# Performance work log

Hardware: AMD Instinct MI355X
Metric: run time of the kernel (lower is better)

Reference implementation:

```python
import jax, jax.numpy as jnp
import numpy as np

PATCH = 5
DIM = 256
HEADS = 8
EPS = 1e-5


def split_patches(t, p):
    # t: [B,H,W,C] -> overlapping patches [B,H,W,p,p,C], stride 1, zero-pad p//2
    pad = p // 2
    tp = jnp.pad(t, ((0, 0), (pad, pad), (pad, pad), (0, 0)))
    H, W = t.shape[1], t.shape[2]
    rows = jnp.arange(H)[:, None] + jnp.arange(p)[None, :]  # [H,p]
    cols = jnp.arange(W)[:, None] + jnp.arange(p)[None, :]  # [W,p]
    return tp[:, rows[:, None, :, None], cols[None, :, None, :], :]


def layernorm(v, g, b):
    mu = jnp.mean(v, axis=-1, keepdims=True)
    var = jnp.var(v, axis=-1, keepdims=True)
    return (v - mu) * jax.lax.rsqrt(var + EPS) * g + b


def mha(q, k, v, w, b, mask):
    # w: [4,D,D] stacked (Wq,Wk,Wv,Wo), b: [4,D]; q:[N,Lq,D], k,v:[N,Lk,D]
    N, Lq, D = q.shape
    dh = D // HEADS
    qh = (q @ w[0] + b[0]).reshape(N, Lq, HEADS, dh)
    kh = (k @ w[1] + b[1]).reshape(N, -1, HEADS, dh)
    vh = (v @ w[2] + b[2]).reshape(N, -1, HEADS, dh)
    sc = jnp.einsum('nqhd,nkhd->nhqk', qh, kh) * (1.0 / float(np.sqrt(dh)))
    if mask is not None:
        sc = jnp.where(mask, sc, jnp.asarray(-1e9, sc.dtype))
    a = jax.nn.softmax(sc, axis=-1)
    o = jnp.einsum('nhqk,nkhd->nqhd', a, vh).reshape(N, Lq, D)
    return o @ w[3] + b[3], a


def setup_inputs() -> dict:
    key = jax.random.key(0)
    ks = jax.random.split(key, 10)
    B, H, W, D = 1, 64, 64, DIM
    x = jax.random.normal(ks[0], (B, H, W, D), dtype=jnp.float32)
    memory = jax.random.normal(ks[1], (B, H, W, D), dtype=jnp.float32)
    active_nodes = jax.random.randint(ks[2], (B, H, W), 0, 2).astype(bool)
    s = 0.05
    return {
        'x': x, 'memory': memory, 'active_nodes': active_nodes,
        'attn_w': jax.random.normal(ks[3], (4, D, D), dtype=jnp.float32) * s,
        'attn_b': jnp.zeros((4, D), dtype=jnp.float32),
        'pattn_w': jax.random.normal(ks[4], (4, D, D), dtype=jnp.float32) * s,
        'pattn_b': jnp.zeros((4, D), dtype=jnp.float32),
        'ff_w1': jax.random.normal(ks[5], (D, 2 * D), dtype=jnp.float32) * s,
        'ff_b1': jnp.zeros((2 * D,), dtype=jnp.float32),
        'ff_w2': jax.random.normal(ks[6], (2 * D, D), dtype=jnp.float32) * s,
        'ff_b2': jnp.zeros((D,), dtype=jnp.float32),
        'ln_g': jnp.ones((3, D), dtype=jnp.float32),   # norm1, norm2, norm3
        'ln_b': jnp.zeros((3, D), dtype=jnp.float32),
    }


def reference(x, memory, active_nodes, attn_w, attn_b, pattn_w, pattn_b,
              ff_w1, ff_b1, ff_w2, ff_b2, ln_g, ln_b):
    B, H, W, D = x.shape
    p = PATCH
    center = p // 2
    L = p * p
    cp = L // 2  # flattened center point

    act = active_nodes[..., None]                      # [B,H,W,1] bool
    ap = split_patches(act, p)                         # [B,H,W,p,p,1]
    # faithful to source: zeroes the entire patch at GRID position (center,center)
    ap = ap.at[:, center, center].set(False)
    wo_center = jnp.any(ap.reshape(B, H, W, L, 1), axis=3)  # [B,H,W,1]
    act = jnp.logical_and(wo_center, act)
    ap = split_patches(act, p)                         # recomputed with updated mask

    xp = split_patches(x, p) * ap                      # zero inactive neighbors
    xp = xp.reshape(B, H, W, L, D)
    mp = split_patches(memory, p).reshape(B, H, W, L, D)
    mask = ap[..., 0].reshape(B, H, W, L)

    N = B * H * W
    keys = xp.reshape(N, L, D)
    mem = mp.reshape(N, L, D)
    q = keys[:, cp:cp + 1, :]                          # [N,1,D]
    m = mask.reshape(N, L)[:, None, None, :]           # [N,1,1,L]

    # EncoderLayer (eval mode: dropout = identity)
    s_, attn = mha(q, keys, keys, attn_w, attn_b, m)
    s = layernorm(q + s_, ln_g[0], ln_b[0])            # norm1
    s_, _ = mha(s, mem, mem, pattn_w, pattn_b, None)
    s = layernorm(s + s_, ln_g[2], ln_b[2])            # norm3
    ff = jax.nn.relu(s @ ff_w1 + ff_b1) @ ff_w2 + ff_b2
    s = layernorm(s + ff, ln_g[1], ln_b[1])            # norm2

    out = jnp.where(act, s[:, 0, :].reshape(B, H, W, D), jnp.asarray(0.0, x.dtype))
    return out, act[..., 0]
```

## Files before the change

### kernel.cpp

```cpp
#include <hip/hip_runtime.h>
#include <math.h>

#define D 256
#define H2 512
#define HEADS 8
#define L 25
#define GH 64
#define GW 64
#define NN 4096
#define EPS 1e-5f
#define SCALE 0.17677669529663687f
#define NND 1048576

typedef __attribute__((ext_vector_type(8))) short short8;
typedef __attribute__((ext_vector_type(4))) float f32x4;

__device__ __forceinline__ bool act_at(const int* __restrict__ active, int h, int w) {
    if (h < 0 || h >= GH || w < 0 || w >= GW) return false;
    if (h == 2 && w == 2) return false;
    return active[h * GW + w] != 0;
}

__device__ __forceinline__ unsigned short f2b(float f) {
    unsigned u = __float_as_uint(f);
    u += 0x7fffu + ((u >> 16) & 1u);
    return (unsigned short)(u >> 16);
}
__device__ __forceinline__ float b2f(short v) {
    return __uint_as_float(((unsigned)(unsigned short)v) << 16);
}

__global__ __launch_bounds__(256)
void prep_kernel(const float* __restrict__ x, const float* __restrict__ mem,
                 const int* __restrict__ active,
                 const float* __restrict__ attn_w, const float* __restrict__ pattn_w,
                 const float* __restrict__ ff_w1, const float* __restrict__ ff_w2,
                 const float* __restrict__ pattn_b,
                 unsigned short* __restrict__ xmB, unsigned short* __restrict__ memB,
                 unsigned short* __restrict__ wB,
                 unsigned short* __restrict__ k2bias, unsigned short* __restrict__ v2bias) {
    const int tid = threadIdx.x;
    const int bid = blockIdx.x;
    if (bid < 192) {
        __shared__ float tile[64][65];
        const float* src; unsigned short* dst;
        int i0, n0, srcLen, dstLen;
        if (bid < 128) {
            int mat = bid >> 4, t16 = bid & 15;
            i0 = (t16 >> 2) * 64; n0 = (t16 & 3) * 64;
            src = (mat < 4) ? (attn_w + mat * 65536) : (pattn_w + (mat - 4) * 65536);
            dst = wB + mat * 65536;
            srcLen = 256; dstLen = 256;
        } else if (bid < 160) {
            int t = bid - 128;
            i0 = (t >> 3) * 64; n0 = (t & 7) * 64;
            src = ff_w1; dst = wB + 524288;
            srcLen = 512; dstLen = 256;
        } else {
            int t = bid - 160;
            i0 = (t >> 2) * 64; n0 = (t & 3) * 64;
            src = ff_w2; dst = wB + 655360;
            srcLen = 256; dstLen = 512;
        }
        int c = tid & 63, r4 = tid >> 6;
        for (int rr = 0; rr < 64; rr += 4)
            tile[rr + r4][c] = src[(size_t)(i0 + rr + r4) * srcLen + n0 + c];
        __syncthreads();
        for (int rr = 0; rr < 64; rr += 4) {
            int r = rr + r4;
            dst[(size_t)(n0 + r) * dstLen + i0 + c] = f2b(tile[c][r]);
        }
    } else {
        const int t0 = (bid - 192) * 256 + tid;
        for (int t = t0; t < 524800; t += 512 * 256) {
            if (t < 262144) {
                int n = t >> 6;
                bool a = act_at(active, n >> 6, n & 63);
                float4 v = ((const float4*)x)[t];
                ushort4 u;
                u.x = f2b(a ? v.x : 0.0f); u.y = f2b(a ? v.y : 0.0f);
                u.z = f2b(a ? v.z : 0.0f); u.w = f2b(a ? v.w : 0.0f);
                ((ushort4*)xmB)[t] = u;
            } else if (t < 524288) {
                int tt = t - 262144;
                float4 v = ((const float4*)mem)[tt];
                ushort4 u;
                u.x = f2b(v.x); u.y = f2b(v.y); u.z = f2b(v.z); u.w = f2b(v.w);
                ((ushort4*)memB)[tt] = u;
            } else {
                int tt = t - 524288;
                if (tt < 256) k2bias[tt] = f2b(pattn_b[256 + tt]);
                else          v2bias[tt - 256] = f2b(pattn_b[512 + (tt - 256)]);
            }
        }
    }
}

__global__ __launch_bounds__(256)
void proj_gemm(const unsigned short* __restrict__ xmB,
               const unsigned short* __restrict__ memB,
               const unsigned short* __restrict__ wB,
               const float* __restrict__ attn_b, const float* __restrict__ pattn_b,
               unsigned short* __restrict__ q1b, unsigned short* __restrict__ k1b,
               unsigned short* __restrict__ v1b, unsigned short* __restrict__ k2b,
               unsigned short* __restrict__ v2b) {
    const int s  = blockIdx.y >> 2;
    const int n0 = (blockIdx.y & 3) * 64;
    const unsigned short* A  = (s < 3) ? xmB : memB;
    const int wtIdx = (s < 3) ? s : (s + 2);
    const unsigned short* WT = wB + (size_t)wtIdx * 65536;
    const float* bias = (s < 3) ? (attn_b + s * 256) : (pattn_b + (s - 2) * 256);
    unsigned short* outB;
    switch (s) { case 0: outB = q1b; break; case 1: outB = k1b; break;
                 case 2: outB = v1b; break; case 3: outB = k2b; break;
                 default: outB = v2b; }

    const int tid = threadIdx.x;
    const int wave = tid >> 6, lane = tid & 63;
    const int m0 = blockIdx.x * 64 + wave * 16;
    const int lr = lane & 15;
    const int lk = (lane >> 4) << 3;
    f32x4 acc[4] = {};
    const unsigned short* arow = A  + (size_t)(m0 + lr) * 256 + lk;
    const unsigned short* brow = WT + (size_t)(n0 + lr) * 256 + lk;
    #pragma unroll
    for (int kk = 0; kk < 256; kk += 32) {
        short8 a = *(const short8*)(arow + kk);
        #pragma unroll
        for (int nf = 0; nf < 4; ++nf) {
            short8 b = *(const short8*)(brow + (size_t)nf * 16 * 256 + kk);
            acc[nf] = __builtin_amdgcn_mfma_f32_16x16x32_bf16(a, b, acc[nf], 0, 0, 0);
        }
    }
    const int rbase = m0 + ((lane >> 4) << 2);
    #pragma unroll
    for (int nf = 0; nf < 4; ++nf) {
        int c = n0 + nf * 16 + lr;
        float bc = bias[c];
        #pragma unroll
        for (int jj = 0; jj < 4; ++jj)
            outB[(size_t)(rbase + jj) * 256 + c] = f2b(acc[nf][jj] + bc);
    }
}

#define KV_OFF   0
#define ACT_OFF  51200
#define WGT_OFF  51328
#define REDA_OFF 64128
#define REDB_OFF 64640
#define STAT_OFF 65152
#define SMEM_SZ  65280
#define T1B_OFF  0
#define SB_OFF   8448
#define HB_OFF   16896

__device__ __forceinline__ void load_union(const unsigned short* __restrict__ base,
                                           int h, int w0, int fallback,
                                           unsigned short (*kvU)[256], int tid) {
    for (int c = tid; c < 3200; c += 512) {
        int u = c >> 5, part = c & 31;
        int r = u / 20;
        int hh = h - 2 + r, ww = w0 - 2 + (u - r * 20);
        bool ib = ((unsigned)hh < GH) && ((unsigned)ww < GW);
        int row = ib ? ((hh << 6) | ww) : fallback;
        *(uint4*)&kvU[u][part * 8] = *(const uint4*)(base + (size_t)row * 256 + part * 8);
    }
}

__global__ __launch_bounds__(512)
void fused_kernel(const int* __restrict__ active, const float* __restrict__ x,
                  const unsigned short* __restrict__ wB,
                  const float* __restrict__ attn_b, const float* __restrict__ pattn_b,
                  const float* __restrict__ ff_b1, const float* __restrict__ ff_b2,
                  const float* __restrict__ ln_g, const float* __restrict__ ln_b,
                  const unsigned short* __restrict__ q1b,
                  const unsigned short* __restrict__ k1b,
                  const unsigned short* __restrict__ v1b,
                  const unsigned short* __restrict__ k2b,
                  const unsigned short* __restrict__ v2b,
                  float* __restrict__ out) {
    const int tid = threadIdx.x;
    const int wv = tid >> 6, lane = tid & 63;
    const int lr = lane & 15, qi = lane >> 4;
    const int bid = ((blockIdx.x & 7) << 5) | (blockIdx.x >> 3);
    const int n0 = bid * 16;
    const int h = n0 >> 6, w0 = n0 & 63;
    const int half = lane >> 5, lam = lane & 31;
    const int m = wv * 2 + half;

    __shared__ __align__(16) char smem[SMEM_SZ];
    unsigned short (*kvU)[256] = (unsigned short(*)[256])(smem + KV_OFF);
    unsigned char* actU        = (unsigned char*)(smem + ACT_OFF);
    float (*wgt)[8][25]        = (float(*)[8][25])(smem + WGT_OFF);
    float (*redA)[8]           = (float(*)[8])(smem + REDA_OFF);
    float (*redB)[8]           = (float(*)[8])(smem + REDB_OFF);
    float (*stats)[2]          = (float(*)[2])(smem + STAT_OFF);
    unsigned short (*T1b)[264] = (unsigned short(*)[264])(smem + T1B_OFF);
    unsigned short (*Sb)[264]  = (unsigned short(*)[264])(smem + SB_OFF);
    unsigned short (*Hb)[520]  = (unsigned short(*)[520])(smem + HB_OFF);

    if (tid < 100) {
        int r = tid / 20;
        int hh = h - 2 + r, ww = w0 - 2 + (tid - r * 20);
        actU[tid] = act_at(active, hh, ww) ? 1 : 0;
    }
    load_union(k1b, h, w0, 0, kvU, tid);
    __syncthreads();

    {
        float q[8];
        short8 qv = *(const short8*)(q1b + (size_t)(n0 + m) * 256 + lam * 8);
        #pragma unroll
        for (int j = 0; j < 8; ++j) q[j] = b2f(qv[j]);
        #pragma unroll 5
        for (int l = 0; l < L; ++l) {
            int u = (l / 5) * 20 + m + (l % 5);
            short8 kv = *(const short8*)&kvU[u][lam * 8];
            float p = q[0] * b2f(kv[0]);
            #pragma unroll
            for (int j = 1; j < 8; ++j) p = fmaf(q[j], b2f(kv[j]), p);
            p += __shfl_xor(p, 1); p += __shfl_xor(p, 2);
            float sv = actU[u] ? p * SCALE : -1e30f;
            if ((lam & 3) == 0) wgt[m][lam >> 2][l] = sv;
        }
    }
    __syncthreads();
    if (tid < 128) {
        int mm = tid >> 3, hd = tid & 7;
        float mx = -1e30f;
        for (int l = 0; l < L; ++l) mx = fmaxf(mx, wgt[mm][hd][l]);
        float sum = 0.0f;
        for (int l = 0; l < L; ++l) { float e = expf(wgt[mm][hd][l] - mx); wgt[mm][hd][l] = e; sum += e; }
        float inv = 1.0f / sum;
        for (int l = 0; l < L; ++l) wgt[mm][hd][l] *= inv;
    }
    __syncthreads();
    load_union(v1b, h, w0, 0, kvU, tid);
    __syncthreads();
    {
        float o[8] = {0.f,0.f,0.f,0.f,0.f,0.f,0.f,0.f};
        #pragma unroll 5
        for (int l = 0; l < L; ++l) {
            int u = (l / 5) * 20 + m + (l % 5);
            if (actU[u]) {
                float wt = wgt[m][lam >> 2][l];
                short8 v8 = *(const short8*)&kvU[u][lam * 8];
                #pragma unroll
                for (int j = 0; j < 8; ++j) o[j] = fmaf(wt, b2f(v8[j]), o[j]);
            }
        }
        __syncthreads();
        unsigned short u8[8];
        #pragma unroll
        for (int j = 0; j < 8; ++j) u8[j] = f2b(o[j]);
        *(uint4*)&T1b[m][lam * 8] = *(uint4*)u8;
    }
    __syncthreads();

    float sreg[2][4];
    {
        const unsigned short* Wo1T = wB + 3 * 65536;
        f32x4 acc[2] = {};
        #pragma unroll
        for (int kk = 0; kk < 256; kk += 32) {
            short8 a = *(const short8*)&T1b[lr][qi * 8 + kk];
            #pragma unroll
            for (int nf = 0; nf < 2; ++nf) {
                short8 b = *(const short8*)(Wo1T + (size_t)(wv * 32 + nf * 16 + lr) * 256 + qi * 8 + kk);
                acc[nf] = __builtin_amdgcn_mfma_f32_16x16x32_bf16(a, b, acc[nf], 0, 0, 0);
            }
        }
        float v[2][4], s1[4] = {0.f,0.f,0.f,0.f}, s2[4] = {0.f,0.f,0.f,0.f};
        #pragma unroll
        for (int nf = 0; nf < 2; ++nf) {
            int c = wv * 32 + nf * 16 + lr;
            float bc = attn_b[768 + c];
            #pragma unroll
            for (int jj = 0; jj < 4; ++jj) {
                int row = n0 + qi * 4 + jj;
                float vv = acc[nf][jj] + bc + x[(size_t)row * D + c];
                v[nf][jj] = vv; s1[jj] += vv; s2[jj] += vv * vv;
            }
        }
        #pragma unroll
        for (int jj = 0; jj < 4; ++jj) {
            #pragma unroll
            for (int off = 1; off < 16; off <<= 1) {
                s1[jj] += __shfl_xor(s1[jj], off);
                s2[jj] += __shfl_xor(s2[jj], off);
            }
        }
        if (lr == 0) {
            #pragma unroll
            for (int jj = 0; jj < 4; ++jj) { redA[qi*4+jj][wv] = s1[jj]; redB[qi*4+jj][wv] = s2[jj]; }
        }
        __syncthreads();
        if (tid < 16) {
            float a1 = 0.f, a2 = 0.f;
            #pragma unroll
            for (int q8 = 0; q8 < 8; ++q8) { a1 += redA[tid][q8]; a2 += redB[tid][q8]; }
            float mu = a1 * (1.0f / D);
            float var = a2 * (1.0f / D) - mu * mu;
            stats[tid][0] = mu; stats[tid][1] = rsqrtf(var + EPS);
        }
        __syncthreads();
        #pragma unroll
        for (int nf = 0; nf < 2; ++nf) {
            int c = wv * 32 + nf * 16 + lr;
            float gg = ln_g[c], bb = ln_b[c];
            #pragma unroll
            for (int jj = 0; jj < 4; ++jj) {
                int ridx = qi * 4 + jj;
                float ov = (v[nf][jj] - stats[ridx][0]) * stats[ridx][1] * gg + bb;
                sreg[nf][jj] = ov;
                Sb[ridx][c] = f2b(ov);
            }
        }
    }
    __syncthreads();

    {
        const unsigned short* Wq2T = wB + 4 * 65536;
        f32x4 acc[2] = {};
        #pragma unroll
        for (int kk = 0; kk < 256; kk += 32) {
            short8 a = *(const short8*)&Sb[lr][qi * 8 + kk];
            #pragma unroll
            for (int nf = 0; nf < 2; ++nf) {
                short8 b = *(const short8*)(Wq2T + (size_t)(wv * 32 + nf * 16 + lr) * 256 + qi * 8 + kk);
                acc[nf] = __builtin_amdgcn_mfma_f32_16x16x32_bf16(a, b, acc[nf], 0, 0, 0);
            }
        }
        __syncthreads();
        #pragma unroll
        for (int nf = 0; nf < 2; ++nf) {
            int c = wv * 32 + nf * 16 + lr;
            float bc = pattn_b[c];
            #pragma unroll
            for (int jj = 0; jj < 4; ++jj)
                T1b[qi * 4 + jj][c] = f2b(acc[nf][jj] + bc);
        }
    }
    __syncthreads();

    float q2[8];
    {
        short8 qv = *(const short8*)&T1b[m][lam * 8];
        #pragma unroll
        for (int j = 0; j < 8; ++j) q2[j] = b2f(qv[j]);
    }
    __syncthreads();
    load_union(k2b, h, w0, NN, kvU, tid);
    __syncthreads();

    #pragma unroll 5
    for (int l = 0; l < L; ++l) {
        int u = (l / 5) * 20 + m + (l % 5);
        short8 kv = *(const short8*)&kvU[u][lam * 8];
        float p = q2[0] * b2f(kv[0]);
        #pragma unroll
        for (int j = 1; j < 8; ++j) p = fmaf(q2[j], b2f(kv[j]), p);
        p += __shfl_xor(p, 1); p += __shfl_xor(p, 2);
        if ((lam & 3) == 0) wgt[m][lam >> 2][l] = p * SCALE;
    }
    __syncthreads();
    if (tid < 128) {
        int mm = tid >> 3, hd = tid & 7;
        float mx = -1e30f;
        for (int l = 0; l < L; ++l) mx = fmaxf(mx, wgt[mm][hd][l]);
        float sum = 0.0f;
        for (int l = 0; l < L; ++l) { float e = expf(wgt[mm][hd][l] - mx); wgt[mm][hd][l] = e; sum += e; }
        float inv = 1.0f / sum;
        for (int l = 0; l < L; ++l) wgt[mm][hd][l] *= inv;
    }
    __syncthreads();
    load_union(v2b, h, w0, NN, kvU, tid);
    __syncthreads();
    {
        float o[8] = {0.f,0.f,0.f,0.f,0.f,0.f,0.f,0.f};
        #pragma unroll 5
        for (int l = 0; l < L; ++l) {
            int u = (l / 5) * 20 + m + (l % 5);
            float wt = wgt[m][lam >> 2][l];
            short8 v8 = *(const short8*)&kvU[u][lam * 8];
            #pragma unroll
            for (int j = 0; j < 8; ++j) o[j] = fmaf(wt, b2f(v8[j]), o[j]);
        }
        __syncthreads();
        unsigned short u8[8];
        #pragma unroll
        for (int j = 0; j < 8; ++j) u8[j] = f2b(o[j]);
        *(uint4*)&T1b[m][lam * 8] = *(uint4*)u8;
    }
    __syncthreads();

    float s2reg[2][4];
    {
        const unsigned short* Wo2T = wB + 7 * 65536;
        f32x4 acc[2] = {};
        #pragma unroll
        for (int kk = 0; kk < 256; kk += 32) {
            short8 a = *(const short8*)&T1b[lr][qi * 8 + kk];
            #pragma unroll
            for (int nf = 0; nf < 2; ++nf) {
                short8 b = *(const short8*)(Wo2T + (size_t)(wv * 32 + nf * 16 + lr) * 256 + qi * 8 + kk);
                acc[nf] = __builtin_amdgcn_mfma_f32_16x16x32_bf16(a, b, acc[nf], 0, 0, 0);
            }
        }
        float v[2][4], s1[4] = {0.f,0.f,0.f,0.f}, s2[4] = {0.f,0.f,0.f,0.f};
        #pragma unroll
        for (int nf = 0; nf < 2; ++nf) {
            int c = wv * 32 + nf * 16 + lr;
            float bc = pattn_b[768 + c];
            #pragma unroll
            for (int jj = 0; jj < 4; ++jj) {
                float vv = acc[nf][jj] + bc + sreg[nf][jj];
                v[nf][jj] = vv; s1[jj] += vv; s2[jj] += vv * vv;
            }
        }
        #pragma unroll
        for (int jj = 0; jj < 4; ++jj) {
            #pragma unroll
            for (int off = 1; off < 16; off <<= 1) {
                s1[jj] += __shfl_xor(s1[jj], off);
                s2[jj] += __shfl_xor(s2[jj], off);
            }
        }
        if (lr == 0) {
            #pragma unroll
            for (int jj = 0; jj < 4; ++jj) { redA[qi*4+jj][wv] = s1[jj]; redB[qi*4+jj][wv] = s2[jj]; }
        }
        __syncthreads();
        if (tid < 16) {
            float a1 = 0.f, a2 = 0.f;
            #pragma unroll
            for (int q8 = 0; q8 < 8; ++q8) { a1 += redA[tid][q8]; a2 += redB[tid][q8]; }
            float mu = a1 * (1.0f / D);
            float var = a2 * (1.0f / D) - mu * mu;
            stats[tid][0] = mu; stats[tid][1] = rsqrtf(var + EPS);
        }
        __syncthreads();
        #pragma unroll
        for (int nf = 0; nf < 2; ++nf) {
            int c = wv * 32 + nf * 16 + lr;
            float gg = ln_g[512 + c], bb = ln_b[512 + c];
            #pragma unroll
            for (int jj = 0; jj < 4; ++jj) {
                int ridx = qi * 4 + jj;
                float ov = (v[nf][jj] - stats[ridx][0]) * stats[ridx][1] * gg + bb;
                s2reg[nf][jj] = ov;
                Sb[ridx][c] = f2b(ov);
            }
        }
    }
    __syncthreads();

    {
        const unsigned short* W1T = wB + 524288;
        f32x4 acc[4] = {};
        #pragma unroll
        for (int kk = 0; kk < 256; kk += 32) {
            short8 a = *(const short8*)&Sb[lr][qi * 8 + kk];
            #pragma unroll
            for (int nf = 0; nf < 4; ++nf) {
                short8 b = *(const short8*)(W1T + (size_t)(wv * 64 + nf * 16 + lr) * 256 + qi * 8 + kk);
                acc[nf] = __builtin_amdgcn_mfma_f32_16x16x32_bf16(a, b, acc[nf], 0, 0, 0);
            }
        }
        #pragma unroll
        for (int nf = 0; nf < 4; ++nf) {
            int c = wv * 64 + nf * 16 + lr;
            float bc = ff_b1[c];
            #pragma unroll
            for (int jj = 0; jj < 4; ++jj)
                Hb[qi * 4 + jj][c] = f2b(fmaxf(acc[nf][jj] + bc, 0.0f));
        }
    }
    __syncthreads();

    {
        const unsigned short* W2T = wB + 655360;
        f32x4 acc[2] = {};
        #pragma unroll
        for (int kk = 0; kk < 512; kk += 32) {
            short8 a = *(const short8*)&Hb[lr][qi * 8 + kk];
            #pragma unroll
            for (int nf = 0; nf < 2; ++nf) {
                short8 b = *(const short8*)(W2T + (size_t)(wv * 32 + nf * 16 + lr) * 512 + qi * 8 + kk);
                acc[nf] = __builtin_amdgcn_mfma_f32_16x16x32_bf16(a, b, acc[nf], 0, 0, 0);
            }
        }
        float v[2][4], s1[4] = {0.f,0.f,0.f,0.f}, s2[4] = {0.f,0.f,0.f,0.f};
        #pragma unroll
        for (int nf = 0; nf < 2; ++nf) {
            int c = wv * 32 + nf * 16 + lr;
            float bc = ff_b2[c];
            #pragma unroll
            for (int jj = 0; jj < 4; ++jj) {
                float vv = acc[nf][jj] + bc + s2reg[nf][jj];
                v[nf][jj] = vv; s1[jj] += vv; s2[jj] += vv * vv;
            }
        }
        #pragma unroll
        for (int jj = 0; jj < 4; ++jj) {
            #pragma unroll
            for (int off = 1; off < 16; off <<= 1) {
                s1[jj] += __shfl_xor(s1[jj], off);
                s2[jj] += __shfl_xor(s2[jj], off);
            }
        }
        if (lr == 0) {
            #pragma unroll
            for (int jj = 0; jj < 4; ++jj) { redA[qi*4+jj][wv] = s1[jj]; redB[qi*4+jj][wv] = s2[jj]; }
        }
        __syncthreads();
        if (tid < 16) {
            float a1 = 0.f, a2 = 0.f;
            #pragma unroll
            for (int q8 = 0; q8 < 8; ++q8) { a1 += redA[tid][q8]; a2 += redB[tid][q8]; }
            float mu = a1 * (1.0f / D);
            float var = a2 * (1.0f / D) - mu * mu;
            stats[tid][0] = mu; stats[tid][1] = rsqrtf(var + EPS);
        }
        __syncthreads();
        bool arow_act[4];
        #pragma unroll
        for (int jj = 0; jj < 4; ++jj) {
            int row = n0 + qi * 4 + jj;
            arow_act[jj] = act_at(active, row >> 6, row & 63);
        }
        #pragma unroll
        for (int nf = 0; nf < 2; ++nf) {
            int c = wv * 32 + nf * 16 + lr;
            float gg = ln_g[256 + c], bb = ln_b[256 + c];
            #pragma unroll
            for (int jj = 0; jj < 4; ++jj) {
                int ridx = qi * 4 + jj;
                float ov = (v[nf][jj] - stats[ridx][0]) * stats[ridx][1] * gg + bb;
                out[(size_t)(n0 + ridx) * D + c] = arow_act[jj] ? ov : 0.0f;
            }
        }
        if (tid < 16) {
            int row = n0 + tid;
            out[(size_t)NND + row] = act_at(active, row >> 6, row & 63) ? 1.0f : 0.0f;
        }
    }
}

extern "C" void kernel_launch(void* const* d_in, const int* in_sizes, int n_in,
                              void* d_out, int out_size, void* d_ws, size_t ws_size,
                              hipStream_t stream) {
    const float* x       = (const float*)d_in[0];
    const float* memory  = (const float*)d_in[1];
    const int*   active  = (const int*)d_in[2];
    const float* attn_w  = (const float*)d_in[3];
    const float* attn_b  = (const float*)d_in[4];
    const float* pattn_w = (const float*)d_in[5];
    const float* pattn_b = (const float*)d_in[6];
    const float* ff_w1   = (const float*)d_in[7];
    const float* ff_b1   = (const float*)d_in[8];
    const float* ff_w2   = (const float*)d_in[9];
    const float* ff_b2   = (const float*)d_in[10];
    const float* ln_g    = (const float*)d_in[11];
    const float* ln_b    = (const float*)d_in[12];
    float* out = (float*)d_out;

    unsigned short* wsb = (unsigned short*)d_ws;
    unsigned short* xmB  = wsb;
    unsigned short* memB = wsb + (size_t)NND;
    unsigned short* wB   = wsb + 2 * (size_t)NND;
    unsigned short* q1b  = wB + 786432;
    unsigned short* k1b  = q1b + (size_t)NND;
    unsigned short* v1b  = k1b + (size_t)NND;
    unsigned short* k2b  = v1b + (size_t)NND;
    unsigned short* v2b  = k2b + (size_t)NND + 256;

    hipLaunchKernelGGL(prep_kernel, dim3(704), dim3(256), 0, stream,
                       x, memory, active, attn_w, pattn_w, ff_w1, ff_w2, pattn_b,
                       xmB, memB, wB, k2b + (size_t)NND, v2b + (size_t)NND);
    hipLaunchKernelGGL(proj_gemm, dim3(64, 20), dim3(256), 0, stream,
                       xmB, memB, wB, attn_b, pattn_b, q1b, k1b, v1b, k2b, v2b);
    hipLaunchKernelGGL(fused_kernel, dim3(256), dim3(512), 0, stream,
                       active, x, wB, attn_b, pattn_b, ff_b1, ff_b2, ln_g, ln_b,
                       q1b, k1b, v1b, k2b, v2b, out);
}
```

Measured before the change: 91.11 us.

## Fuse bf16 input conversion into projection GEMM and halve fused-kernel rows per block

Drops the prep pass that converted x and memory to bf16 (with masking) and instead converts fp32 inputs to bf16 inside the projection GEMM's A-operand load. This removes one full read-write round trip of both activations through memory, at the cost of reading fp32 directly, which doubles A-load bytes and repeats the conversion for each of the 4 column-tile blocks. The fused kernel now uses 8 query rows per block with 256 threads and 512 blocks, giving smaller shared-memory neighbour windows (60 rows instead of 100) and more blocks. The 16-row MFMA tiles are now half empty, with rows duplicated and masked on store, so matrix work is wasted.

```diff
diff --git a/kernel.cpp b/kernel.cpp
--- a/kernel.cpp
+++ b/kernel.cpp
@@ -11,6 +11,8 @@
 #define EPS 1e-5f
 #define SCALE 0.17677669529663687f
 #define NND 1048576
+#define ROWS 8
+#define UN 60
 
 typedef __attribute__((ext_vector_type(8))) short short8;
 typedef __attribute__((ext_vector_type(4))) float f32x4;
@@ -31,12 +33,9 @@
 }
 
 __global__ __launch_bounds__(256)
-void prep_kernel(const float* __restrict__ x, const float* __restrict__ mem,
-                 const int* __restrict__ active,
-                 const float* __restrict__ attn_w, const float* __restrict__ pattn_w,
+void prep_kernel(const float* __restrict__ attn_w, const float* __restrict__ pattn_w,
                  const float* __restrict__ ff_w1, const float* __restrict__ ff_w2,
                  const float* __restrict__ pattn_b,
-                 unsigned short* __restrict__ xmB, unsigned short* __restrict__ memB,
                  unsigned short* __restrict__ wB,
                  unsigned short* __restrict__ k2bias, unsigned short* __restrict__ v2bias) {
     const int tid = threadIdx.x;
@@ -71,34 +70,16 @@
             dst[(size_t)(n0 + r) * dstLen + i0 + c] = f2b(tile[c][r]);
         }
     } else {
-        const int t0 = (bid - 192) * 256 + tid;
-        for (int t = t0; t < 524800; t += 512 * 256) {
-            if (t < 262144) {
-                int n = t >> 6;
-                bool a = act_at(active, n >> 6, n & 63);
-                float4 v = ((const float4*)x)[t];
-                ushort4 u;
-                u.x = f2b(a ? v.x : 0.0f); u.y = f2b(a ? v.y : 0.0f);
-                u.z = f2b(a ? v.z : 0.0f); u.w = f2b(a ? v.w : 0.0f);
-                ((ushort4*)xmB)[t] = u;
-            } else if (t < 524288) {
-                int tt = t - 262144;
-                float4 v = ((const float4*)mem)[tt];
-                ushort4 u;
-                u.x = f2b(v.x); u.y = f2b(v.y); u.z = f2b(v.z); u.w = f2b(v.w);
-                ((ushort4*)memB)[tt] = u;
-            } else {
-                int tt = t - 524288;
-                if (tt < 256) k2bias[tt] = f2b(pattn_b[256 + tt]);
-                else          v2bias[tt - 256] = f2b(pattn_b[512 + (tt - 256)]);
-            }
+        if (tid < 256) {
+            k2bias[tid] = f2b(pattn_b[256 + tid]);
+            v2bias[tid] = f2b(pattn_b[512 + tid]);
         }
     }
 }
 
 __global__ __launch_bounds__(256)
-void proj_gemm(const unsigned short* __restrict__ xmB,
-               const unsigned short* __restrict__ memB,
+void proj_gemm(const float* __restrict__ x, const float* __restrict__ mem,
+               const int* __restrict__ active,
                const unsigned short* __restrict__ wB,
                const float* __restrict__ attn_b, const float* __restrict__ pattn_b,
                unsigned short* __restrict__ q1b, unsigned short* __restrict__ k1b,
@@ -106,7 +87,8 @@
                unsigned short* __restrict__ v2b) {
     const int s  = blockIdx.y >> 2;
     const int n0 = (blockIdx.y & 3) * 64;
-    const unsigned short* A  = (s < 3) ? xmB : memB;
+    const float* Asrc = (s < 3) ? x : mem;
+    const bool useMask = (s < 3);
     const int wtIdx = (s < 3) ? s : (s + 2);
     const unsigned short* WT = wB + (size_t)wtIdx * 65536;
     const float* bias = (s < 3) ? (attn_b + s * 256) : (pattn_b + (s - 2) * 256);
@@ -120,12 +102,25 @@
     const int m0 = blockIdx.x * 64 + wave * 16;
     const int lr = lane & 15;
     const int lk = (lane >> 4) << 3;
+    const int arowIdx = m0 + lr;
+    const bool rowAct = !useMask || act_at(active, arowIdx >> 6, arowIdx & 63);
+
     f32x4 acc[4] = {};
-    const unsigned short* arow = A  + (size_t)(m0 + lr) * 256 + lk;
+    const float* arow = Asrc + (size_t)arowIdx * 256 + lk;
     const unsigned short* brow = WT + (size_t)(n0 + lr) * 256 + lk;
     #pragma unroll
     for (int kk = 0; kk < 256; kk += 32) {
-        short8 a = *(const short8*)(arow + kk);
+        float4 a0 = *(const float4*)(arow + kk);
+        float4 a1 = *(const float4*)(arow + kk + 4);
+        short8 a;
+        a[0] = rowAct ? (short)f2b(a0.x) : (short)0;
+        a[1] = rowAct ? (short)f2b(a0.y) : (short)0;
+        a[2] = rowAct ? (short)f2b(a0.z) : (short)0;
+        a[3] = rowAct ? (short)f2b(a0.w) : (short)0;
+        a[4] = rowAct ? (short)f2b(a1.x) : (short)0;
+        a[5] = rowAct ? (short)f2b(a1.y) : (short)0;
+        a[6] = rowAct ? (short)f2b(a1.z) : (short)0;
+        a[7] = rowAct ? (short)f2b(a1.w) : (short)0;
         #pragma unroll
         for (int nf = 0; nf < 4; ++nf) {
             short8 b = *(const short8*)(brow + (size_t)nf * 16 * 256 + kk);
@@ -144,30 +139,30 @@
 }
 
 #define KV_OFF   0
-#define ACT_OFF  51200
-#define WGT_OFF  51328
-#define REDA_OFF 64128
-#define REDB_OFF 64640
-#define STAT_OFF 65152
-#define SMEM_SZ  65280
+#define ACT_OFF  30720
+#define WGT_OFF  30784
+#define REDA_OFF 37184
+#define REDB_OFF 37440
+#define STAT_OFF 37696
+#define SMEM_SZ  37824
 #define T1B_OFF  0
 #define SB_OFF   8448
 #define HB_OFF   16896
 
-__device__ __forceinline__ void load_union(const unsigned short* __restrict__ base,
-                                           int h, int w0, int fallback,
-                                           unsigned short (*kvU)[256], int tid) {
-    for (int c = tid; c < 3200; c += 512) {
+__device__ __forceinline__ void load_union60(const unsigned short* __restrict__ base,
+                                             int h, int w0, int fallback,
+                                             unsigned short (*kvU)[256], int tid) {
+    for (int c = tid; c < UN * 32; c += 256) {
         int u = c >> 5, part = c & 31;
-        int r = u / 20;
-        int hh = h - 2 + r, ww = w0 - 2 + (u - r * 20);
+        int r = u / 12, cc = u - r * 12;
+        int hh = h - 2 + r, ww = w0 - 2 + cc;
         bool ib = ((unsigned)hh < GH) && ((unsigned)ww < GW);
         int row = ib ? ((hh << 6) | ww) : fallback;
         *(uint4*)&kvU[u][part * 8] = *(const uint4*)(base + (size_t)row * 256 + part * 8);
     }
 }
 
-__global__ __launch_bounds__(512)
+__global__ __launch_bounds__(256)
 void fused_kernel(const int* __restrict__ active, const float* __restrict__ x,
                   const unsigned short* __restrict__ wB,
                   const float* __restrict__ attn_b, const float* __restrict__ pattn_b,
@@ -182,29 +177,29 @@
     const int tid = threadIdx.x;
     const int wv = tid >> 6, lane = tid & 63;
     const int lr = lane & 15, qi = lane >> 4;
-    const int bid = ((blockIdx.x & 7) << 5) | (blockIdx.x >> 3);
-    const int n0 = bid * 16;
-    const int h = n0 >> 6, w0 = n0 & 63;
     const int half = lane >> 5, lam = lane & 31;
     const int m = wv * 2 + half;
+    const int bid = ((blockIdx.x & 7) << 6) | (blockIdx.x >> 3);
+    const int n0 = bid * ROWS;
+    const int h = n0 >> 6, w0 = n0 & 63;
 
     __shared__ __align__(16) char smem[SMEM_SZ];
     unsigned short (*kvU)[256] = (unsigned short(*)[256])(smem + KV_OFF);
     unsigned char* actU        = (unsigned char*)(smem + ACT_OFF);
     float (*wgt)[8][25]        = (float(*)[8][25])(smem + WGT_OFF);
-    float (*redA)[8]           = (float(*)[8])(smem + REDA_OFF);
-    float (*redB)[8]           = (float(*)[8])(smem + REDB_OFF);
+    float (*redA)[4]           = (float(*)[4])(smem + REDA_OFF);
+    float (*redB)[4]           = (float(*)[4])(smem + REDB_OFF);
     float (*stats)[2]          = (float(*)[2])(smem + STAT_OFF);
     unsigned short (*T1b)[264] = (unsigned short(*)[264])(smem + T1B_OFF);
     unsigned short (*Sb)[264]  = (unsigned short(*)[264])(smem + SB_OFF);
     unsigned short (*Hb)[520]  = (unsigned short(*)[520])(smem + HB_OFF);
 
-    if (tid < 100) {
-        int r = tid / 20;
-        int hh = h - 2 + r, ww = w0 - 2 + (tid - r * 20);
+    if (tid < UN) {
+        int r = tid / 12;
+        int hh = h - 2 + r, ww = w0 - 2 + (tid - r * 12);
         actU[tid] = act_at(active, hh, ww) ? 1 : 0;
     }
-    load_union(k1b, h, w0, 0, kvU, tid);
+    load_union60(k1b, h, w0, 0, kvU, tid);
     __syncthreads();
 
     {
@@ -214,7 +209,7 @@
         for (int j = 0; j < 8; ++j) q[j] = b2f(qv[j]);
         #pragma unroll 5
         for (int l = 0; l < L; ++l) {
-            int u = (l / 5) * 20 + m + (l % 5);
+            int u = (l / 5) * 12 + m + (l % 5);
             short8 kv = *(const short8*)&kvU[u][lam * 8];
             float p = q[0] * b2f(kv[0]);
             #pragma unroll
@@ -225,7 +220,7 @@
         }
     }
     __syncthreads();
-    if (tid < 128) {
+    if (tid < 64) {
         int mm = tid >> 3, hd = tid & 7;
         float mx = -1e30f;
         for (int l = 0; l < L; ++l) mx = fmaxf(mx, wgt[mm][hd][l]);
@@ -235,13 +230,13 @@
         for (int l = 0; l < L; ++l) wgt[mm][hd][l] *= inv;
     }
     __syncthreads();
-    load_union(v1b, h, w0, 0, kvU, tid);
+    load_union60(v1b, h, w0, 0, kvU, tid);
     __syncthreads();
     {
         float o[8] = {0.f,0.f,0.f,0.f,0.f,0.f,0.f,0.f};
         #pragma unroll 5
         for (int l = 0; l < L; ++l) {
-            int u = (l / 5) * 20 + m + (l % 5);
+            int u = (l / 5) * 12 + m + (l % 5);
             if (actU[u]) {
                 float wt = wgt[m][lam >> 2][l];
                 short8 v8 = *(const short8*)&kvU[u][lam * 8];
@@ -257,28 +252,29 @@
     }
     __syncthreads();
 
-    float sreg[2][4];
+    float sreg[4][4];
     {
         const unsigned short* Wo1T = wB + 3 * 65536;
-        f32x4 acc[2] = {};
+        f32x4 acc[4] = {};
         #pragma unroll
         for (int kk = 0; kk < 256; kk += 32) {
             short8 a = *(const short8*)&T1b[lr][qi * 8 + kk];
             #pragma unroll
-            for (int nf = 0; nf < 2; ++nf) {
-                short8 b = *(const short8*)(Wo1T + (size_t)(wv * 32 + nf * 16 + lr) * 256 + qi * 8 + kk);
+            for (int nf = 0; nf < 4; ++nf) {
+                short8 b = *(const short8*)(Wo1T + (size_t)(wv * 64 + nf * 16 + lr) * 256 + qi * 8 + kk);
                 acc[nf] = __builtin_amdgcn_mfma_f32_16x16x32_bf16(a, b, acc[nf], 0, 0, 0);
             }
         }
-        float v[2][4], s1[4] = {0.f,0.f,0.f,0.f}, s2[4] = {0.f,0.f,0.f,0.f};
-        #pragma unroll
-        for (int nf = 0; nf < 2; ++nf) {
-            int c = wv * 32 + nf * 16 + lr;
+        float v[4][4], s1[4] = {0.f,0.f,0.f,0.f}, s2[4] = {0.f,0.f,0.f,0.f};
+        #pragma unroll
+        for (int nf = 0; nf < 4; ++nf) {
+            int c = wv * 64 + nf * 16 + lr;
             float bc = attn_b[768 + c];
             #pragma unroll
             for (int jj = 0; jj < 4; ++jj) {
-                int row = n0 + qi * 4 + jj;
-                float vv = acc[nf][jj] + bc + x[(size_t)row * D + c];
+                int ridx = qi * 4 + jj;
+                float xr = x[(size_t)(n0 + (ridx & 7)) * D + c];
+                float vv = acc[nf][jj] + bc + xr;
                 v[nf][jj] = vv; s1[jj] += vv; s2[jj] += vv * vv;
             }
         }
@@ -296,17 +292,16 @@
         }
         __syncthreads();
         if (tid < 16) {
-            float a1 = 0.f, a2 = 0.f;
-            #pragma unroll
-            for (int q8 = 0; q8 < 8; ++q8) { a1 += redA[tid][q8]; a2 += redB[tid][q8]; }
+            float a1 = redA[tid][0]+redA[tid][1]+redA[tid][2]+redA[tid][3];
+            float a2 = redB[tid][0]+redB[tid][1]+redB[tid][2]+redB[tid][3];
             float mu = a1 * (1.0f / D);
             float var = a2 * (1.0f / D) - mu * mu;
             stats[tid][0] = mu; stats[tid][1] = rsqrtf(var + EPS);
         }
         __syncthreads();
         #pragma unroll
-        for (int nf = 0; nf < 2; ++nf) {
-            int c = wv * 32 + nf * 16 + lr;
+        for (int nf = 0; nf < 4; ++nf) {
+            int c = wv * 64 + nf * 16 + lr;
             float gg = ln_g[c], bb = ln_b[c];
             #pragma unroll
             for (int jj = 0; jj < 4; ++jj) {
@@ -321,20 +316,20 @@
 
     {
         const unsigned short* Wq2T = wB + 4 * 65536;
-        f32x4 acc[2] = {};
+        f32x4 acc[4] = {};
         #pragma unroll
         for (int kk = 0; kk < 256; kk += 32) {
             short8 a = *(const short8*)&Sb[lr][qi * 8 + kk];
             #pragma unroll
-            for (int nf = 0; nf < 2; ++nf) {
-                short8 b = *(const short8*)(Wq2T + (size_t)(wv * 32 + nf * 16 + lr) * 256 + qi * 8 + kk);
+            for (int nf = 0; nf < 4; ++nf) {
+                short8 b = *(const short8*)(Wq2T + (size_t)(wv * 64 + nf * 16 + lr) * 256 + qi * 8 + kk);
                 acc[nf] = __builtin_amdgcn_mfma_f32_16x16x32_bf16(a, b, acc[nf], 0, 0, 0);
             }
         }
         __syncthreads();
         #pragma unroll
-        for (int nf = 0; nf < 2; ++nf) {
-            int c = wv * 32 + nf * 16 + lr;
+        for (int nf = 0; nf < 4; ++nf) {
+            int c = wv * 64 + nf * 16 + lr;
             float bc = pattn_b[c];
             #pragma unroll
             for (int jj = 0; jj < 4; ++jj)
@@ -350,12 +345,12 @@
         for (int j = 0; j < 8; ++j) q2[j] = b2f(qv[j]);
     }
     __syncthreads();
-    load_union(k2b, h, w0, NN, kvU, tid);
+    load_union60(k2b, h, w0, NN, kvU, tid);
     __syncthreads();
 
     #pragma unroll 5
     for (int l = 0; l < L; ++l) {
-        int u = (l / 5) * 20 + m + (l % 5);
+        int u = (l / 5) * 12 + m + (l % 5);
         short8 kv = *(const short8*)&kvU[u][lam * 8];
         float p = q2[0] * b2f(kv[0]);
         #pragma unroll
@@ -364,7 +359,7 @@
         if ((lam & 3) == 0) wgt[m][lam >> 2][l] = p * SCALE;
     }
     __syncthreads();
-    if (tid < 128) {
+    if (tid < 64) {
         int mm = tid >> 3, hd = tid & 7;
         float mx = -1e30f;
         for (int l = 0; l < L; ++l) mx = fmaxf(mx, wgt[mm][hd][l]);
@@ -374,13 +369,13 @@
         for (int l = 0; l < L; ++l) wgt[mm][hd][l] *= inv;
     }
     __syncthreads();
-    load_union(v2b, h, w0, NN, kvU, tid);
+    load_union60(v2b, h, w0, NN, kvU, tid);
     __syncthreads();
     {
         float o[8] = {0.f,0.f,0.f,0.f,0.f,0.f,0.f,0.f};
         #pragma unroll 5
         for (int l = 0; l < L; ++l) {
-            int u = (l / 5) * 20 + m + (l % 5);
+            int u = (l / 5) * 12 + m + (l % 5);
             float wt = wgt[m][lam >> 2][l];
             short8 v8 = *(const short8*)&kvU[u][lam * 8];
             #pragma unroll
@@ -394,23 +389,23 @@
     }
     __syncthreads();
 
-    float s2reg[2][4];
+    float s2reg[4][4];
     {
         const unsigned short* Wo2T = wB + 7 * 65536;
-        f32x4 acc[2] = {};
+        f32x4 acc[4] = {};
         #pragma unroll
         for (int kk = 0; kk < 256; kk += 32) {
             short8 a = *(const short8*)&T1b[lr][qi * 8 + kk];
             #pragma unroll
-            for (int nf = 0; nf < 2; ++nf) {
-                short8 b = *(const short8*)(Wo2T + (size_t)(wv * 32 + nf * 16 + lr) * 256 + qi * 8 + kk);
+            for (int nf = 0; nf < 4; ++nf) {
+                short8 b = *(const short8*)(Wo2T + (size_t)(wv * 64 + nf * 16 + lr) * 256 + qi * 8 + kk);
                 acc[nf] = __builtin_amdgcn_mfma_f32_16x16x32_bf16(a, b, acc[nf], 0, 0, 0);
             }
         }
-        float v[2][4], s1[4] = {0.f,0.f,0.f,0.f}, s2[4] = {0.f,0.f,0.f,0.f};
-        #pragma unroll
-        for (int nf = 0; nf < 2; ++nf) {
-            int c = wv * 32 + nf * 16 + lr;
+        float v[4][4], s1[4] = {0.f,0.f,0.f,0.f}, s2[4] = {0.f,0.f,0.f,0.f};
+        #pragma unroll
+        for (int nf = 0; nf < 4; ++nf) {
+            int c = wv * 64 + nf * 16 + lr;
             float bc = pattn_b[768 + c];
             #pragma unroll
             for (int jj = 0; jj < 4; ++jj) {
@@ -432,17 +427,16 @@
         }
         __syncthreads();
         if (tid < 16) {
-            float a1 = 0.f, a2 = 0.f;
-            #pragma unroll
-            for (int q8 = 0; q8 < 8; ++q8) { a1 += redA[tid][q8]; a2 += redB[tid][q8]; }
+            float a1 = redA[tid][0]+redA[tid][1]+redA[tid][2]+redA[tid][3];
+            float a2 = redB[tid][0]+redB[tid][1]+redB[tid][2]+redB[tid][3];
             float mu = a1 * (1.0f / D);
             float var = a2 * (1.0f / D) - mu * mu;
             stats[tid][0] = mu; stats[tid][1] = rsqrtf(var + EPS);
         }
         __syncthreads();
         #pragma unroll
-        for (int nf = 0; nf < 2; ++nf) {
-            int c = wv * 32 + nf * 16 + lr;
+        for (int nf = 0; nf < 4; ++nf) {
+            int c = wv * 64 + nf * 16 + lr;
             float gg = ln_g[512 + c], bb = ln_b[512 + c];
             #pragma unroll
             for (int jj = 0; jj < 4; ++jj) {
@@ -457,19 +451,19 @@
 
     {
         const unsigned short* W1T = wB + 524288;
-        f32x4 acc[4] = {};
+        f32x4 acc[8] = {};
         #pragma unroll
         for (int kk = 0; kk < 256; kk += 32) {
             short8 a = *(const short8*)&Sb[lr][qi * 8 + kk];
             #pragma unroll
-            for (int nf = 0; nf < 4; ++nf) {
-                short8 b = *(const short8*)(W1T + (size_t)(wv * 64 + nf * 16 + lr) * 256 + qi * 8 + kk);
+            for (int nf = 0; nf < 8; ++nf) {
+                short8 b = *(const short8*)(W1T + (size_t)(wv * 128 + nf * 16 + lr) * 256 + qi * 8 + kk);
                 acc[nf] = __builtin_amdgcn_mfma_f32_16x16x32_bf16(a, b, acc[nf], 0, 0, 0);
             }
         }
         #pragma unroll
-        for (int nf = 0; nf < 4; ++nf) {
-            int c = wv * 64 + nf * 16 + lr;
+        for (int nf = 0; nf < 8; ++nf) {
+            int c = wv * 128 + nf * 16 + lr;
             float bc = ff_b1[c];
             #pragma unroll
             for (int jj = 0; jj < 4; ++jj)
@@ -480,20 +474,20 @@
 
     {
         const unsigned short* W2T = wB + 655360;
-        f32x4 acc[2] = {};
+        f32x4 acc[4] = {};
         #pragma unroll
         for (int kk = 0; kk < 512; kk += 32) {
             short8 a = *(const short8*)&Hb[lr][qi * 8 + kk];
             #pragma unroll
-            for (int nf = 0; nf < 2; ++nf) {
-                short8 b = *(const short8*)(W2T + (size_t)(wv * 32 + nf * 16 + lr) * 512 + qi * 8 + kk);
+            for (int nf = 0; nf < 4; ++nf) {
+                short8 b = *(const short8*)(W2T + (size_t)(wv * 64 + nf * 16 + lr) * 512 + qi * 8 + kk);
                 acc[nf] = __builtin_amdgcn_mfma_f32_16x16x32_bf16(a, b, acc[nf], 0, 0, 0);
             }
         }
-        float v[2][4], s1[4] = {0.f,0.f,0.f,0.f}, s2[4] = {0.f,0.f,0.f,0.f};
-        #pragma unroll
-        for (int nf = 0; nf < 2; ++nf) {
-            int c = wv * 32 + nf * 16 + lr;
+        float v[4][4], s1[4] = {0.f,0.f,0.f,0.f}, s2[4] = {0.f,0.f,0.f,0.f};
+        #pragma unroll
+        for (int nf = 0; nf < 4; ++nf) {
+            int c = wv * 64 + nf * 16 + lr;
             float bc = ff_b2[c];
             #pragma unroll
             for (int jj = 0; jj < 4; ++jj) {
@@ -515,32 +509,29 @@
         }
         __syncthreads();
         if (tid < 16) {
-            float a1 = 0.f, a2 = 0.f;
-            #pragma unroll
-            for (int q8 = 0; q8 < 8; ++q8) { a1 += redA[tid][q8]; a2 += redB[tid][q8]; }
+            float a1 = redA[tid][0]+redA[tid][1]+redA[tid][2]+redA[tid][3];
+            float a2 = redB[tid][0]+redB[tid][1]+redB[tid][2]+redB[tid][3];
             float mu = a1 * (1.0f / D);
             float var = a2 * (1.0f / D) - mu * mu;
             stats[tid][0] = mu; stats[tid][1] = rsqrtf(var + EPS);
         }
         __syncthreads();
-        bool arow_act[4];
-        #pragma unroll
-        for (int jj = 0; jj < 4; ++jj) {
-            int row = n0 + qi * 4 + jj;
-            arow_act[jj] = act_at(active, row >> 6, row & 63);
-        }
-        #pragma unroll
-        for (int nf = 0; nf < 2; ++nf) {
-            int c = wv * 32 + nf * 16 + lr;
+        #pragma unroll
+        for (int nf = 0; nf < 4; ++nf) {
+            int c = wv * 64 + nf * 16 + lr;
             float gg = ln_g[256 + c], bb = ln_b[256 + c];
             #pragma unroll
             for (int jj = 0; jj < 4; ++jj) {
                 int ridx = qi * 4 + jj;
-                float ov = (v[nf][jj] - stats[ridx][0]) * stats[ridx][1] * gg + bb;
-                out[(size_t)(n0 + ridx) * D + c] = arow_act[jj] ? ov : 0.0f;
-            }
-        }
-        if (tid < 16) {
+                if (ridx < ROWS) {
+                    int row = n0 + ridx;
+                    bool a = act_at(active, row >> 6, row & 63);
+                    float ov = (v[nf][jj] - stats[ridx][0]) * stats[ridx][1] * gg + bb;
+                    out[(size_t)row * D + c] = a ? ov : 0.0f;
+                }
+            }
+        }
+        if (tid < ROWS) {
             int row = n0 + tid;
             out[(size_t)NND + row] = act_at(active, row >> 6, row & 63) ? 1.0f : 0.0f;
         }
@@ -566,21 +557,20 @@
     float* out = (float*)d_out;
 
     unsigned short* wsb = (unsigned short*)d_ws;
-    unsigned short* xmB  = wsb;
-    unsigned short* memB = wsb + (size_t)NND;
-    unsigned short* wB   = wsb + 2 * (size_t)NND;
+    unsigned short* wB   = wsb;
     unsigned short* q1b  = wB + 786432;
     unsigned short* k1b  = q1b + (size_t)NND;
     unsigned short* v1b  = k1b + (size_t)NND;
     unsigned short* k2b  = v1b + (size_t)NND;
     unsigned short* v2b  = k2b + (size_t)NND + 256;
 
-    hipLaunchKernelGGL(prep_kernel, dim3(704), dim3(256), 0, stream,
-                       x, memory, active, attn_w, pattn_w, ff_w1, ff_w2, pattn_b,
-                       xmB, memB, wB, k2b + (size_t)NND, v2b + (size_t)NND);
+    hipLaunchKernelGGL(prep_kernel, dim3(193), dim3(256), 0, stream,
+                       attn_w, pattn_w, ff_w1, ff_w2, pattn_b,
+                       wB, k2b + (size_t)NND, v2b + (size_t)NND);
     hipLaunchKernelGGL(proj_gemm, dim3(64, 20), dim3(256), 0, stream,
-                       xmB, memB, wB, attn_b, pattn_b, q1b, k1b, v1b, k2b, v2b);
-    hipLaunchKernelGGL(fused_kernel, dim3(256), dim3(512), 0, stream,
+                       x, memory, active, wB, attn_b, pattn_b,
+                       q1b, k1b, v1b, k2b, v2b);
+    hipLaunchKernelGGL(fused_kernel, dim3(512), dim3(256), 0, stream,
                        active, x, wB, attn_b, pattn_b, ff_b1, ff_b2, ln_g, ln_b,
                        q1b, k1b, v1b, k2b, v2b, out);
 }
```

After: 129.0 us. 41.6% more time.
